# Kernel tuning notes

Measured on AMD Instinct MI355X. Metric: run time of the kernel, lower is better.

Reference implementation:

```python
import jax, jax.numpy as jnp
import numpy as np

EMBED_DIM = 1024
NUM_HEADS = 16
BATCH = 4
SEQ = 2048
HEAD_DIM = EMBED_DIM // NUM_HEADS


def get_alibi_slope(num_heads):
    x = (2 ** 8) ** (1 / num_heads)
    slope = jnp.array([1 / x ** (i + 1) for i in range(num_heads)], dtype=jnp.float32)
    return slope[:, None, None]  # [H,1,1]


def setup_inputs() -> dict:
    key = jax.random.key(0)
    k1, k2, k3 = jax.random.split(key, 3)
    x = jax.random.normal(k1, (BATCH, SEQ, EMBED_DIM), dtype=jnp.float32)
    # causal mask, broadcastable to [B,H,S,S]
    mask = jnp.tril(jnp.ones((SEQ, SEQ), dtype=bool))[None, None, :, :]
    W_qkv = jax.random.normal(k2, (EMBED_DIM, 3 * EMBED_DIM), dtype=jnp.float32) * (EMBED_DIM ** -0.5)
    b_qkv = jnp.zeros((3 * EMBED_DIM,), dtype=jnp.float32)
    W_out = jax.random.normal(k3, (EMBED_DIM, EMBED_DIM), dtype=jnp.float32) * (EMBED_DIM ** -0.5)
    b_out = jnp.zeros((EMBED_DIM,), dtype=jnp.float32)
    return {"x": x, "mask": mask, "W_qkv": W_qkv, "b_qkv": b_qkv, "W_out": W_out, "b_out": b_out}


def reference(x, mask, W_qkv, b_qkv, W_out, b_out):
    B, S, E = x.shape
    H, D = NUM_HEADS, HEAD_DIM
    qkv = x @ W_qkv + b_qkv                     # [B,S,3E]
    qkv = qkv.reshape(B, S, 3, H, D)
    q, k, v = qkv[:, :, 0], qkv[:, :, 1], qkv[:, :, 2]  # each [B,S,H,D]
    scores = jnp.einsum('bqhd,bkhd->bhqk', q, k) / jnp.sqrt(jnp.asarray(D, x.dtype))
    # ALiBi bias: slope[h] * (k_pos - q_pos)
    rel = (jnp.arange(S)[None, :] - jnp.arange(S)[:, None]).astype(x.dtype)  # [S,S]
    scores = scores + get_alibi_slope(H).astype(x.dtype) * rel               # broadcast [H,S,S]
    scores = jnp.where(mask, scores, jnp.asarray(-1e9, x.dtype))
    attn = jax.nn.softmax(scores, axis=-1)       # [B,H,S,S]
    out = jnp.einsum('bhqk,bkhd->bqhd', attn, v).reshape(B, S, E)
    return out @ W_out + b_out
```

## Files before the change

### kernel.cpp

```cpp
#include <hip/hip_runtime.h>
#include <hip/hip_bf16.h>
#include <cstdint>
#include <cstddef>

#define BATCH  4
#define SEQ    2048
#define EMBED  1024
#define NHEADS 16
#define HDIM   64

typedef __attribute__((ext_vector_type(8))) short  short8;
typedef __attribute__((ext_vector_type(4))) float  floatx4;

#define MASK_NEG (-1.0e30f)
#define LOG2E    1.44269504f

__device__ __forceinline__ float bf2f(ushort u) {
  union { uint32_t i; float f; } v; v.i = ((uint32_t)u) << 16; return v.f;
}
__device__ __forceinline__ ushort f2bf(float f) {
  union { float f; uint32_t i; } v; v.f = f;
  uint32_t u = v.i;
  return (ushort)((u + 0x7fffu + ((u >> 16) & 1u)) >> 16);
}
__device__ __forceinline__ uint32_t f2bf_pk(float a, float b) {
  union { __hip_bfloat162 h; uint32_t u; } v;
  v.h = __float22bfloat162_rn(make_float2(a, b));
  return v.u;
}
__device__ __forceinline__ float fast_exp2(float x) {
  float r;
  asm("v_exp_f32 %0, %1" : "=v"(r) : "v"(x));
  return r;
}
__device__ __forceinline__ floatx4 max4(floatx4 a, floatx4 b) {
  floatx4 r;
  r[0] = fmaxf(a[0], b[0]); r[1] = fmaxf(a[1], b[1]);
  r[2] = fmaxf(a[2], b[2]); r[3] = fmaxf(a[3], b[3]);
  return r;
}
__device__ __forceinline__ void gll16(const ushort* g, ushort* l) {
  __builtin_amdgcn_global_load_lds(
      (const __attribute__((address_space(1))) void*)g,
      (__attribute__((address_space(3))) void*)l, 16, 0, 0);
}

__global__ __launch_bounds__(256) void detect_dtype(
    const uint32_t* __restrict__ x, int* __restrict__ flag) {
  __shared__ int sh[256];
  int tid = threadIdx.x;
  int c = 0;
#pragma unroll
  for (int i = 0; i < 16; i++) {
    uint32_t w = x[tid * 16 + i];
    uint32_t lo = w & 0xFFFFu;
    int e = (int)((lo >> 7) & 0xFF);
    if (lo == 0u || (e >= 100 && e <= 140)) c++;
  }
  sh[tid] = c;
  __syncthreads();
  if (tid == 0) {
    int s = 0;
    for (int i = 0; i < 256; i++) s += sh[i];
    *flag = (s >= 3500) ? 1 : 0;
  }
}

__global__ __launch_bounds__(256) void cvt_bf16_v4(
    const void* __restrict__ in, ushort* __restrict__ out,
    const int* __restrict__ flag, int n4) {
  bool isbf = (*flag != 0);
  int stride = gridDim.x * 256;
  for (int i = blockIdx.x * 256 + threadIdx.x; i < n4; i += stride) {
    if (isbf) {
      ((uint2*)out)[i] = ((const uint2*)in)[i];
    } else {
      float4 f = ((const float4*)in)[i];
      uint2 o;
      o.x = f2bf_pk(f.x, f.y);
      o.y = f2bf_pk(f.z, f.w);
      ((uint2*)out)[i] = o;
    }
  }
}

__global__ __launch_bounds__(256) void cvt_biases(
    const void* __restrict__ bq, const void* __restrict__ bo,
    ushort* __restrict__ bqb, ushort* __restrict__ bob,
    const int* __restrict__ flag) {
  bool isbf = (*flag != 0);
  int i = blockIdx.x * 256 + threadIdx.x;
  if (i < 3 * EMBED) {
    bqb[i] = isbf ? ((const ushort*)bq)[i] : f2bf(((const float*)bq)[i]);
  } else {
    int j = i - 3 * EMBED;
    bob[j] = isbf ? ((const ushort*)bo)[j] : f2bf(((const float*)bo)[j]);
  }
}

__global__ __launch_bounds__(256) void transpose_cvt(
    const void* __restrict__ in, ushort* __restrict__ out,
    const int* __restrict__ flag, int R, int C) {
  bool isbf = (*flag != 0);
  __shared__ ushort tile[32][33];
  int bx = blockIdx.x * 32;
  int by = blockIdx.y * 32;
  int tx = threadIdx.x & 31, ty = threadIdx.x >> 5;
#pragma unroll
  for (int i = 0; i < 32; i += 8) {
    size_t idx = (size_t)(by + ty + i) * C + bx + tx;
    tile[ty + i][tx] = isbf ? ((const ushort*)in)[idx] : f2bf(((const float*)in)[idx]);
  }
  __syncthreads();
#pragma unroll
  for (int i = 0; i < 32; i += 8)
    out[(size_t)(bx + ty + i) * R + by + tx] = tile[tx][ty + i];
}

__global__ __launch_bounds__(256) void transpose_v(
    const ushort* __restrict__ in, ushort* __restrict__ out) {
  __shared__ ushort tile[32][33];
  int bh = blockIdx.z;
  int s0 = blockIdx.x * 32;
  int d0 = blockIdx.y * 32;
  int tx = threadIdx.x & 31, ty = threadIdx.x >> 5;
  const ushort* ip = in + (size_t)bh * SEQ * HDIM;
  ushort* op = out + (size_t)bh * SEQ * HDIM;
#pragma unroll
  for (int i = 0; i < 32; i += 8)
    tile[ty + i][tx] = ip[(size_t)(s0 + ty + i) * HDIM + d0 + tx];
  __syncthreads();
#pragma unroll
  for (int i = 0; i < 32; i += 8)
    op[(size_t)(d0 + ty + i) * SEQ + s0 + tx] = tile[tx][ty + i];
}

template <int EPI>
__global__ __launch_bounds__(256) void gemm128(
    const ushort* __restrict__ A, const ushort* __restrict__ BT,
    const ushort* __restrict__ bias,
    ushort* __restrict__ out0, ushort* __restrict__ out1, ushort* __restrict__ out2,
    const int* __restrict__ flag,
    int M, int N, int K) {
  __shared__ __align__(16) ushort Al[128 * 64];
  __shared__ __align__(16) ushort Bl[128 * 64];

  const int tid  = threadIdx.x;
  const int lane = tid & 63, wave = tid >> 6;
  const int quad = lane >> 4, l15 = lane & 15;
  const int wm = wave >> 1, wn = wave & 1;
  const int rowA0 = blockIdx.y * 128;
  const int colB0 = blockIdx.x * 128;

  floatx4 acc[4][4] = {};

  int srow[4], sc8[4];
#pragma unroll
  for (int j = 0; j < 4; j++) {
    int s = tid + j * 256;
    srow[j] = s >> 3;
    sc8[j] = ((s & 7) ^ (srow[j] & 7)) * 8;
  }

  for (int kk = 0; kk < K; kk += 64) {
    __syncthreads();
#pragma unroll
    for (int j = 0; j < 4; j++)
      gll16(&A[(size_t)(rowA0 + srow[j]) * K + kk + sc8[j]], &Al[(tid + j * 256) * 8]);
#pragma unroll
    for (int j = 0; j < 4; j++)
      gll16(&BT[(size_t)(colB0 + srow[j]) * K + kk + sc8[j]], &Bl[(tid + j * 256) * 8]);
    __syncthreads();

#pragma unroll
    for (int h = 0; h < 2; h++) {
      short8 af[4], bf[4];
#pragma unroll
      for (int mt = 0; mt < 4; mt++) {
        int row = wm * 64 + mt * 16 + l15;
        int pos = (quad + 4 * h) ^ (l15 & 7);
        af[mt] = *(const short8*)&Al[row * 64 + pos * 8];
      }
#pragma unroll
      for (int nt = 0; nt < 4; nt++) {
        int row = wn * 64 + nt * 16 + l15;
        int pos = (quad + 4 * h) ^ (l15 & 7);
        bf[nt] = *(const short8*)&Bl[row * 64 + pos * 8];
      }
#pragma unroll
      for (int mt = 0; mt < 4; mt++)
#pragma unroll
        for (int nt = 0; nt < 4; nt++)
          acc[mt][nt] = __builtin_amdgcn_mfma_f32_16x16x32_bf16(af[mt], bf[nt], acc[mt][nt], 0, 0, 0);
    }
  }

  const bool isbf = (EPI == 1) ? (*flag != 0) : true;

#pragma unroll
  for (int mt = 0; mt < 4; mt++)
#pragma unroll
    for (int nt = 0; nt < 4; nt++)
#pragma unroll
      for (int r = 0; r < 4; r++) {
        int row = rowA0 + wm * 64 + mt * 16 + quad * 4 + r;
        int col = colB0 + wn * 64 + nt * 16 + l15;
        float v = acc[mt][nt][r] + bf2f(bias[col]);
        if (EPI == 0) {
          int three = col >> 10, rem = col & 1023, h = rem >> 6, d = rem & 63;
          int b = row >> 11, s = row & 2047;
          ushort* dst = (three == 0) ? out0 : (three == 1) ? out1 : out2;
          dst[((size_t)(b * NHEADS + h) * SEQ + s) * HDIM + d] = f2bf(v);
        } else {
          if (isbf) out0[(size_t)row * N + col] = f2bf(v);
          else      ((float*)out0)[(size_t)row * N + col] = v;
        }
      }
}

__global__ __launch_bounds__(256, 4) void attn_kernel(
    const ushort* __restrict__ Q, const ushort* __restrict__ K,
    const ushort* __restrict__ VT, ushort* __restrict__ Oout) {
  __shared__ __align__(16) ushort Kl[2][64 * 64];
  __shared__ __align__(16) ushort Vt[2][64 * 64];
  __shared__ __align__(16) ushort Pl[4][16 * 64];

  const int tid  = threadIdx.x;
  const int lane = tid & 63, wave = tid >> 6;
  const int quad = lane >> 4, l15 = lane & 15;

  const int L   = blockIdx.x + 16 * blockIdx.y + 256 * blockIdx.z;
  const int xcd = L & 7;
  const int idx = L >> 3;
  const int bh  = xcd * 8 + (idx >> 4);
  const int p   = idx & 15;
  const int h   = bh & 15, b = bh >> 4;

  const ushort* Qp  = Q  + (size_t)bh * SEQ * HDIM;
  const ushort* Kp  = K  + (size_t)bh * SEQ * HDIM;
  const ushort* VTp = VT + (size_t)bh * SEQ * HDIM;

  const float slope2 = exp2f(-0.5f * (float)(h + 1)) * LOG2E;
  const float c2 = 0.125f * LOG2E;

  floatx4 ab[4];
#pragma unroll
  for (int kct = 0; kct < 4; kct++)
#pragma unroll
    for (int r = 0; r < 4; r++)
      ab[kct][r] = slope2 * (float)(kct * 16 + quad * 4 + r);

  const int sr0 = tid >> 3;
  const int scc = ((tid & 7) ^ (sr0 & 7)) * 8;
  const int sxr = l15 & 7;

#define STAGE(KB, BUF)                                                        \
  do {                                                                        \
    gll16(&Kp[(size_t)((KB) + sr0) * HDIM + scc],       &Kl[BUF][tid * 8]);   \
    gll16(&Kp[(size_t)((KB) + sr0 + 32) * HDIM + scc],  &Kl[BUF][tid * 8 + 2048]); \
    gll16(&VTp[(size_t)sr0 * SEQ + (KB) + scc],         &Vt[BUF][tid * 8]);   \
    gll16(&VTp[(size_t)(sr0 + 32) * SEQ + (KB) + scc],  &Vt[BUF][tid * 8 + 2048]); \
  } while (0)

#define ATTN_TILE(KB, CUR, MASKED)                                            \
  do {                                                                        \
    floatx4 w[4];                                                             \
    _Pragma("unroll")                                                         \
    for (int kct = 0; kct < 4; kct++) {                                       \
      const ushort* kr = &Kl[CUR][(kct * 16 + l15) * 64];                     \
      short8 a0 = *(const short8*)&kr[(quad ^ sxr) * 8];                      \
      short8 a1 = *(const short8*)&kr[((quad + 4) ^ sxr) * 8];                \
      floatx4 z = {};                                                         \
      z = __builtin_amdgcn_mfma_f32_16x16x32_bf16(a0, qf0, z, 0, 0, 0);       \
      z = __builtin_amdgcn_mfma_f32_16x16x32_bf16(a1, qf1, z, 0, 0, 0);       \
      w[kct] = z * c2 + ab[kct];                                              \
    }                                                                         \
    if (MASKED) {                                                             \
      const float qrel = qrowf - (float)(KB);                                 \
      _Pragma("unroll")                                                       \
      for (int kct = 0; kct < 4; kct++)                                       \
        _Pragma("unroll")                                                     \
        for (int r = 0; r < 4; r++)                                           \
          if ((float)(kct * 16 + quad * 4 + r) > qrel) w[kct][r] = MASK_NEG;  \
    }                                                                         \
    floatx4 wm4 = max4(max4(w[0], w[1]), max4(w[2], w[3]));                   \
    float mloc = fmaxf(fmaxf(wm4[0], wm4[1]), fmaxf(wm4[2], wm4[3]));         \
    mloc = fmaxf(mloc, __shfl_xor(mloc, 16, 64));                             \
    mloc = fmaxf(mloc, __shfl_xor(mloc, 32, 64));                             \
    const float bk = slope2 * (float)(KB);                                    \
    const float mlt = mloc + bk;                                              \
    const unsigned long long g = __ballot(mlt > m2 + 8.0f);                   \
    float al = 1.0f;                                                          \
    if (g) {                                                                  \
      float mn = fmaxf(m2, mlt);                                              \
      al = fast_exp2(m2 - mn);                                                \
      m2 = mn;                                                                \
    }                                                                         \
    const float mnb = m2 - bk;                                                \
    float rs = 0.f;                                                           \
    _Pragma("unroll")                                                         \
    for (int kct = 0; kct < 4; kct++) {                                       \
      float p0 = fast_exp2(w[kct][0] - mnb);                                  \
      float p1 = fast_exp2(w[kct][1] - mnb);                                  \
      float p2 = fast_exp2(w[kct][2] - mnb);                                  \
      float p3 = fast_exp2(w[kct][3] - mnb);                                  \
      rs += (p0 + p1) + (p2 + p3);                                            \
      uint2 pw;                                                               \
      pw.x = f2bf_pk(p0, p1);                                                 \
      pw.y = f2bf_pk(p2, p3);                                                 \
      *(uint2*)&Pl[wave][l15 * 64 + ((kct * 2 + (quad >> 1)) ^ sxr) * 8 +     \
                         (quad & 1) * 4] = pw;                                \
    }                                                                         \
    if (g) {                                                                  \
      floatx4 alrv;                                                           \
      _Pragma("unroll")                                                       \
      for (int r = 0; r < 4; r++) alrv[r] = __shfl(al, quad * 4 + r, 16);     \
      _Pragma("unroll")                                                       \
      for (int ct = 0; ct < 4; ct++) o_acc[ct] *= alrv;                       \
      li = li * al + rs;                                                      \
    } else {                                                                  \
      li += rs;                                                               \
    }                                                                         \
    _Pragma("unroll")                                                         \
    for (int ks = 0; ks < 2; ks++) {                                          \
      short8 vf[4];                                                           \
      _Pragma("unroll")                                                       \
      for (int ct = 0; ct < 4; ct++)                                          \
        vf[ct] = *(const short8*)&Vt[CUR][(ct * 16 + l15) * 64 +              \
                                          ((ks * 4 + quad) ^ sxr) * 8];       \
      short8 pf = *(const short8*)&Pl[wave][l15 * 64 +                        \
                                            ((ks * 4 + quad) ^ sxr) * 8];     \
      _Pragma("unroll")                                                       \
      for (int ct = 0; ct < 4; ct++)                                          \
        o_acc[ct] = __builtin_amdgcn_mfma_f32_16x16x32_bf16(pf, vf[ct],       \
                                                            o_acc[ct], 0, 0, 0); \
    }                                                                         \
  } while (0)

  for (int qsel = 0; qsel < 2; qsel++) {
    const int qt  = qsel ? (31 - p) : p;
    const int wq0 = qt * 64 + wave * 16;

    short8 qf0, qf1;
    {
      const ushort* qr = &Qp[(size_t)(wq0 + l15) * HDIM];
      qf0 = *(const short8*)&qr[quad * 8];
      qf1 = *(const short8*)&qr[32 + quad * 8];
    }

    float m2 = MASK_NEG, li = 0.f;
    const float qrowf = (float)(wq0 + l15);
    floatx4 o_acc[4] = {};

    __syncthreads();
    STAGE(0, 0);
    __syncthreads();

    const int last = qt;
    for (int kt = 0; kt < last; kt++) {
      const int cur = kt & 1;
      STAGE((kt + 1) * 64, cur ^ 1);
      ATTN_TILE(kt * 64, cur, 0);
      __syncthreads();
    }

    ATTN_TILE(last * 64, last & 1, 1);

    {
      float lif = li + __shfl_xor(li, 16, 64);
      lif += __shfl_xor(lif, 32, 64);
      float inv = 1.0f / fmaxf(lif, 1e-20f);
      float invr[4];
#pragma unroll
      for (int r = 0; r < 4; r++) invr[r] = __shfl(inv, quad * 4 + r, 16);
#pragma unroll
      for (int ct = 0; ct < 4; ct++)
#pragma unroll
        for (int r = 0; r < 4; r++) {
          int q = wq0 + quad * 4 + r;
          float v = o_acc[ct][r] * invr[r];
          Oout[(size_t)(b * SEQ + q) * EMBED + h * HDIM + ct * 16 + l15] = f2bf(v);
        }
    }
  }
#undef ATTN_TILE
#undef STAGE
}

extern "C" void kernel_launch(void* const* d_in, const int* in_sizes, int n_in,
                              void* d_out, int out_size, void* d_ws, size_t ws_size,
                              hipStream_t stream) {
  const void* x     = d_in[0];
  const void* W_qkv = d_in[2];
  const void* b_qkv = d_in[3];
  const void* W_out = d_in[4];
  const void* b_out = d_in[5];

  char* ws = (char*)d_ws;
  int*    flag = (int*)(ws + 0);
  ushort* xb   = (ushort*)(ws + 1024);
  ushort* WTq  = (ushort*)(ws + 16778240);
  ushort* WTo  = (ushort*)(ws + 23069696);
  ushort* bqb  = (ushort*)(ws + 25166848);
  ushort* bob  = (ushort*)(ws + 25172992);
  ushort* Kw   = (ushort*)(ws + 25175040);
  ushort* Vw   = (ushort*)(ws + 41952256);
  ushort* VTw  = (ushort*)(ws + 58729472);
  ushort* Aw   = Vw;
  ushort* Qw   = (ws_size >= (size_t)75506688 + 16777216)
                   ? (ushort*)(ws + 75506688)
                   : (ushort*)d_out;

  detect_dtype<<<1, 256, 0, stream>>>((const uint32_t*)x, flag);

  cvt_bf16_v4<<<2048, 256, 0, stream>>>(x, xb, flag, BATCH * SEQ * EMBED / 4);
  cvt_biases<<<16, 256, 0, stream>>>(b_qkv, b_out, bqb, bob, flag);

  transpose_cvt<<<dim3(3072 / 32, 1024 / 32), 256, 0, stream>>>(W_qkv, WTq, flag, 1024, 3072);
  transpose_cvt<<<dim3(1024 / 32, 1024 / 32), 256, 0, stream>>>(W_out, WTo, flag, 1024, 1024);

  gemm128<0><<<dim3(3072 / 128, 8192 / 128), 256, 0, stream>>>(
      xb, WTq, bqb, Qw, Kw, Vw, flag, BATCH * SEQ, 3 * EMBED, EMBED);

  transpose_v<<<dim3(SEQ / 32, HDIM / 32, BATCH * NHEADS), 256, 0, stream>>>(Vw, VTw);

  attn_kernel<<<dim3(16, 16, 4), 256, 0, stream>>>(Qw, Kw, VTw, Aw);

  gemm128<1><<<dim3(1024 / 128, 8192 / 128), 256, 0, stream>>>(
      Aw, WTo, bob, (ushort*)d_out, nullptr, nullptr, flag, BATCH * SEQ, EMBED, EMBED);
}
```

Before: 295.0 us.

## Keep softmax probabilities in registers by permuting K rows to match MFMA layout

After: 288.9 us. 1.02x faster.

```diff
diff --git a/kernel.cpp b/kernel.cpp
--- a/kernel.cpp
+++ b/kernel.cpp
@@ -11,6 +11,7 @@
 
 typedef __attribute__((ext_vector_type(8))) short  short8;
 typedef __attribute__((ext_vector_type(4))) float  floatx4;
+typedef __attribute__((ext_vector_type(4))) unsigned int uintx4;
 
 #define MASK_NEG (-1.0e30f)
 #define LOG2E    1.44269504f
@@ -223,7 +224,6 @@
     const ushort* __restrict__ VT, ushort* __restrict__ Oout) {
   __shared__ __align__(16) ushort Kl[2][64 * 64];
   __shared__ __align__(16) ushort Vt[2][64 * 64];
-  __shared__ __align__(16) ushort Pl[4][16 * 64];
 
   const int tid  = threadIdx.x;
   const int lane = tid & 63, wave = tid >> 6;
@@ -248,11 +248,18 @@
   for (int kct = 0; kct < 4; kct++)
 #pragma unroll
     for (int r = 0; r < 4; r++)
-      ab[kct][r] = slope2 * (float)(kct * 16 + quad * 4 + r);
+      ab[kct][r] = slope2 * (float)((kct & 1) * 32 + quad * 8 + (kct >> 1) * 4 + r);
+  const float q8f = (float)(quad * 8);
 
   const int sr0 = tid >> 3;
-  const int scc = ((tid & 7) ^ (sr0 & 7)) * 8;
-  const int sxr = l15 & 7;
+  const int fS  = (sr0 & 3) | (((sr0 >> 3) & 1) << 2);
+  const int scc = ((tid & 7) ^ fS) * 8;
+
+  const int fK  = (l15 & 3) | (((l15 >> 2) & 1) << 2);
+  const int fV  = (l15 & 3) | (((l15 >> 3) & 1) << 2);
+  const int cA  = quad ^ fK;
+  const int cV0 = quad ^ fV;
+  const int kRowB = (l15 >> 2) * 8 + (l15 & 3);
 
 #define STAGE(KB, BUF)                                                        \
   do {                                                                        \
@@ -267,21 +274,22 @@
     floatx4 w[4];                                                             \
     _Pragma("unroll")                                                         \
     for (int kct = 0; kct < 4; kct++) {                                       \
-      const ushort* kr = &Kl[CUR][(kct * 16 + l15) * 64];                     \
-      short8 a0 = *(const short8*)&kr[(quad ^ sxr) * 8];                      \
-      short8 a1 = *(const short8*)&kr[((quad + 4) ^ sxr) * 8];                \
+      const ushort* kr = &Kl[CUR][(kRowB + (kct & 1) * 32 + (kct >> 1) * 4) * 64]; \
+      short8 a0 = *(const short8*)&kr[cA * 8];                                \
+      short8 a1 = *(const short8*)&kr[(cA ^ 4) * 8];                          \
       floatx4 z = {};                                                         \
       z = __builtin_amdgcn_mfma_f32_16x16x32_bf16(a0, qf0, z, 0, 0, 0);       \
       z = __builtin_amdgcn_mfma_f32_16x16x32_bf16(a1, qf1, z, 0, 0, 0);       \
       w[kct] = z * c2 + ab[kct];                                              \
     }                                                                         \
     if (MASKED) {                                                             \
-      const float qrel = qrowf - (float)(KB);                                 \
+      const float qrel = qrowf - (float)(KB) - q8f;                           \
       _Pragma("unroll")                                                       \
       for (int kct = 0; kct < 4; kct++)                                       \
         _Pragma("unroll")                                                     \
         for (int r = 0; r < 4; r++)                                           \
-          if ((float)(kct * 16 + quad * 4 + r) > qrel) w[kct][r] = MASK_NEG;  \
+          if ((float)((kct & 1) * 32 + (kct >> 1) * 4 + r) > qrel)            \
+            w[kct][r] = MASK_NEG;                                             \
     }                                                                         \
     floatx4 wm4 = max4(max4(w[0], w[1]), max4(w[2], w[3]));                   \
     float mloc = fmaxf(fmaxf(wm4[0], wm4[1]), fmaxf(wm4[2], wm4[3]));         \
@@ -298,6 +306,7 @@
     }                                                                         \
     const float mnb = m2 - bk;                                                \
     float rs = 0.f;                                                           \
+    uintx4 pa0 = {}, pa1 = {};                                                \
     _Pragma("unroll")                                                         \
     for (int kct = 0; kct < 4; kct++) {                                       \
       float p0 = fast_exp2(w[kct][0] - mnb);                                  \
@@ -305,11 +314,13 @@
       float p2 = fast_exp2(w[kct][2] - mnb);                                  \
       float p3 = fast_exp2(w[kct][3] - mnb);                                  \
       rs += (p0 + p1) + (p2 + p3);                                            \
-      uint2 pw;                                                               \
-      pw.x = f2bf_pk(p0, p1);                                                 \
-      pw.y = f2bf_pk(p2, p3);                                                 \
-      *(uint2*)&Pl[wave][l15 * 64 + ((kct * 2 + (quad >> 1)) ^ sxr) * 8 +     \
-                         (quad & 1) * 4] = pw;                                \
+      if (kct & 1) {                                                          \
+        pa1[(kct >> 1) * 2]     = f2bf_pk(p0, p1);                            \
+        pa1[(kct >> 1) * 2 + 1] = f2bf_pk(p2, p3);                            \
+      } else {                                                                \
+        pa0[(kct >> 1) * 2]     = f2bf_pk(p0, p1);                            \
+        pa0[(kct >> 1) * 2 + 1] = f2bf_pk(p2, p3);                            \
+      }                                                                       \
     }                                                                         \
     if (g) {                                                                  \
       floatx4 alrv;                                                           \
@@ -321,19 +332,15 @@
     } else {                                                                  \
       li += rs;                                                               \
     }                                                                         \
+    const short8 pf0 = __builtin_bit_cast(short8, pa0);                       \
+    const short8 pf1 = __builtin_bit_cast(short8, pa1);                       \
     _Pragma("unroll")                                                         \
-    for (int ks = 0; ks < 2; ks++) {                                          \
-      short8 vf[4];                                                           \
-      _Pragma("unroll")                                                       \
-      for (int ct = 0; ct < 4; ct++)                                          \
-        vf[ct] = *(const short8*)&Vt[CUR][(ct * 16 + l15) * 64 +              \
-                                          ((ks * 4 + quad) ^ sxr) * 8];       \
-      short8 pf = *(const short8*)&Pl[wave][l15 * 64 +                        \
-                                            ((ks * 4 + quad) ^ sxr) * 8];     \
-      _Pragma("unroll")                                                       \
-      for (int ct = 0; ct < 4; ct++)                                          \
-        o_acc[ct] = __builtin_amdgcn_mfma_f32_16x16x32_bf16(pf, vf[ct],       \
-                                                            o_acc[ct], 0, 0, 0); \
+    for (int ct = 0; ct < 4; ct++) {                                          \
+      const ushort* vr = &Vt[CUR][(ct * 16 + l15) * 64];                      \
+      short8 vf0 = *(const short8*)&vr[cV0 * 8];                              \
+      short8 vf1 = *(const short8*)&vr[(cV0 ^ 4) * 8];                        \
+      o_acc[ct] = __builtin_amdgcn_mfma_f32_16x16x32_bf16(pf0, vf0, o_acc[ct], 0, 0, 0); \
+      o_acc[ct] = __builtin_amdgcn_mfma_f32_16x16x32_bf16(pf1, vf1, o_acc[ct], 0, 0, 0); \
     }                                                                         \
   } while (0)
 
```
